# Kernel tuning notes

Measured on AMD Instinct MI355X. Metric: run time of the kernel, lower is better.

## Reference

```python
import jax, jax.numpy as jnp
import numpy as np

N_NODES = 100000


def sage_conv(x, src, dst, W_l, W_r, b):
    """PyG SAGEConv with mean aggregation: lin_l(mean_{j in N(i)} x_j) + lin_r(x_i) + b."""
    n = x.shape[0]
    msg = jax.ops.segment_sum(x[src], dst, num_segments=n)          # [N, C] sum of neighbor feats
    deg = jax.ops.segment_sum(jnp.ones_like(src, dtype=x.dtype), dst, num_segments=n)  # [N]
    agg = msg / jnp.maximum(deg, 1.0)[:, None]                      # mean aggregate
    return agg @ W_l + x @ W_r + b


def setup_inputs() -> dict:
    key = jax.random.key(0)
    ks = jax.random.split(key, 10)
    in_ch, hid, out_ch = 128, 128, 1
    E = 640000
    scale_in = 1.0 / np.sqrt(in_ch)
    scale_h = 1.0 / np.sqrt(hid)
    return {
        "x": jax.random.normal(ks[0], (N_NODES, in_ch), dtype=jnp.float32),
        "edge_index": jax.random.randint(ks[1], (2, E), 0, N_NODES, dtype=jnp.int64),
        "W1l": jax.random.normal(ks[2], (in_ch, hid), dtype=jnp.float32) * scale_in,
        "W1r": jax.random.normal(ks[3], (in_ch, hid), dtype=jnp.float32) * scale_in,
        "b1": jnp.zeros((hid,), dtype=jnp.float32),
        "W2l": jax.random.normal(ks[4], (hid, hid), dtype=jnp.float32) * scale_h,
        "W2r": jax.random.normal(ks[5], (hid, hid), dtype=jnp.float32) * scale_h,
        "b2": jnp.zeros((hid,), dtype=jnp.float32),
        "Wfc": jax.random.normal(ks[6], (hid, out_ch), dtype=jnp.float32) * scale_h,
        "bfc": jnp.zeros((out_ch,), dtype=jnp.float32),
    }


def reference(x, edge_index, W1l, W1r, b1, W2l, W2r, b2, Wfc, bfc):
    src, dst = edge_index[0], edge_index[1]
    h = sage_conv(x, src, dst, W1l, W1r, b1)
    h = jax.nn.relu(h)
    # dropout p=0.2 is identity in eval mode (training=False)
    h = sage_conv(h, src, dst, W2l, W2r, b2)
    h = jax.nn.relu(h)
    return jax.nn.sigmoid(h @ Wfc + bfc)
```

## Files before the change

### kernel.cpp

```cpp
#include <hip/hip_runtime.h>
#include <cstdint>

#define NN 100000
#define CH 128
#define NT_BLK 32
#define SCAN_B 256

typedef __bf16 bf16x8 __attribute__((ext_vector_type(8)));
typedef __bf16 bf16x4 __attribute__((ext_vector_type(4)));
typedef float  f32x4  __attribute__((ext_vector_type(4)));

__device__ __forceinline__ float b2f(unsigned short u) {
    union { unsigned int i; float f; } v; v.i = ((unsigned int)u) << 16; return v.f;
}


__global__ void k_count(const int* __restrict__ dst, int* __restrict__ cnt, int E) {
    int e = blockIdx.x * blockDim.x + threadIdx.x;
    if (e < E) atomicAdd(&cnt[dst[e]], 1);
}

__global__ void k_scan_block(const int* __restrict__ cnt, int* __restrict__ rowptr,
                             int* __restrict__ bsum, int n) {
    __shared__ int tmp[SCAN_B];
    int i = blockIdx.x * SCAN_B + threadIdx.x;
    int v = (i < n) ? cnt[i] : 0;
    tmp[threadIdx.x] = v;
    __syncthreads();
    for (int off = 1; off < SCAN_B; off <<= 1) {
        int t = (threadIdx.x >= off) ? tmp[threadIdx.x - off] : 0;
        __syncthreads();
        tmp[threadIdx.x] += t;
        __syncthreads();
    }
    if (i < n) rowptr[i] = tmp[threadIdx.x] - v;
    if (threadIdx.x == SCAN_B - 1) bsum[blockIdx.x] = tmp[SCAN_B - 1];
}

__global__ void k_scan_add(int* __restrict__ rowptr, const int* __restrict__ bsum,
                           int* __restrict__ cursor, int n, int E) {
    __shared__ int sd[SCAN_B];
    const int t = threadIdx.x;
    int s = 0;
    for (int j = t; j < (int)blockIdx.x; j += SCAN_B) s += bsum[j];
    sd[t] = s;
    __syncthreads();
    for (int off = SCAN_B / 2; off > 0; off >>= 1) {
        if (t < off) sd[t] += sd[t + off];
        __syncthreads();
    }
    const int base = sd[0];
    int i = blockIdx.x * SCAN_B + t;
    if (i < n) {
        int v = rowptr[i] + base;
        rowptr[i] = v;
        cursor[i] = v;
    }
    if (i == 0) rowptr[n] = E;
}

__global__ void k_fill(const int* __restrict__ src, const int* __restrict__ dst,
                       int* __restrict__ cursor, int* __restrict__ csr, int E) {
    int e = blockIdx.x * blockDim.x + threadIdx.x;
    if (e >= E) return;
    int slot = atomicAdd(&cursor[dst[e]], 1);
    csr[slot] = src[e];
}

__global__ void k_wconv(const float* __restrict__ W1l, const float* __restrict__ W1r,
                        const float* __restrict__ W2l, const float* __restrict__ W2r,
                        __bf16* __restrict__ wB) {
    int tid = blockIdx.x * blockDim.x + threadIdx.x;
    int l    = tid >> 12;
    int rem  = tid & 4095;
    int kt   = rem >> 9;
    int nt   = (rem >> 6) & 7;
    int lane = rem & 63;
    const float* Wl = l ? W2l : W1l;
    const float* Wr = l ? W2r : W1r;
    int n  = nt * 16 + (lane & 15);
    int k0 = kt * 32 + (lane >> 4) * 8;
    bf16x8 v;
#pragma unroll
    for (int i = 0; i < 8; ++i) {
        int k = k0 + i;
        float f = (k < CH) ? Wl[k * CH + n] : Wr[(k - CH) * CH + n];
        v[i] = (__bf16)f;
    }
    *reinterpret_cast<bf16x8*>(wB + (size_t)tid * 8) = v;
}

template<bool FC, typename FT>
__global__ __launch_bounds__(256) void k_layer(
    const FT* __restrict__ feat,
    const int* __restrict__ rowptr, const int* __restrict__ csr,
    const bf16x8* __restrict__ wfrag,
    const float* __restrict__ bias,
    const float* __restrict__ Wfc, const float* __restrict__ bfc,
    void* __restrict__ outv)
{
    __shared__ unsigned short a_lds[NT_BLK * 256];
    __shared__ float red[4][16];
    char* lb = (char*)a_lds;
    const int tid = threadIdx.x;
    const int node0 = blockIdx.x * NT_BLK;

    const int g = tid >> 5;
    const int q = tid & 31;

    auto loadrow = [&](int idx) -> float4 {
        if constexpr (sizeof(FT) == 2) {
            const ushort4 u = *reinterpret_cast<const ushort4*>(
                (const unsigned short*)feat + (size_t)idx * CH + q * 4);
            return make_float4(b2f(u.x), b2f(u.y), b2f(u.z), b2f(u.w));
        } else {
            return *reinterpret_cast<const float4*>((const float*)feat + (size_t)idx * CH + q * 4);
        }
    };

#pragma unroll
    for (int it = 0; it < NT_BLK / 8; ++it) {
        const int r = it * 8 + g;
        const int node = node0 + r;
        const int swz = (r & 7) << 4;
        float4 s = make_float4(0.f, 0.f, 0.f, 0.f);
        bf16x4 k2 = {(__bf16)0.f, (__bf16)0.f, (__bf16)0.f, (__bf16)0.f};
        if (node < NN) {
            const int r0 = rowptr[node], r1 = rowptr[node + 1];
            int rr = r0;
            for (; rr + 4 <= r1; rr += 4) {
                const int i0 = csr[rr], i1 = csr[rr + 1], i2 = csr[rr + 2], i3 = csr[rr + 3];
                const float4 v0 = loadrow(i0), v1 = loadrow(i1), v2 = loadrow(i2), v3 = loadrow(i3);
                s.x += (v0.x + v1.x) + (v2.x + v3.x);
                s.y += (v0.y + v1.y) + (v2.y + v3.y);
                s.z += (v0.z + v1.z) + (v2.z + v3.z);
                s.w += (v0.w + v1.w) + (v2.w + v3.w);
            }
            for (; rr < r1; ++rr) {
                const float4 v = loadrow(csr[rr]);
                s.x += v.x; s.y += v.y; s.z += v.z; s.w += v.w;
            }
            const float invd = 1.0f / fmaxf((float)(r1 - r0), 1.0f);
            s.x *= invd; s.y *= invd; s.z *= invd; s.w *= invd;
            if constexpr (sizeof(FT) == 2) {
                const ushort4 u = *reinterpret_cast<const ushort4*>(
                    (const unsigned short*)feat + (size_t)node * CH + q * 4);
                k2 = *reinterpret_cast<const bf16x4*>(&u);
            } else {
                const float4 sv = *reinterpret_cast<const float4*>((const float*)feat + (size_t)node * CH + q * 4);
                k2[0] = (__bf16)sv.x; k2[1] = (__bf16)sv.y; k2[2] = (__bf16)sv.z; k2[3] = (__bf16)sv.w;
            }
        }
        bf16x4 a;
        a[0] = (__bf16)s.x; a[1] = (__bf16)s.y; a[2] = (__bf16)s.z; a[3] = (__bf16)s.w;
        *reinterpret_cast<bf16x4*>(lb + r * 512 + ((q * 8) ^ swz)) = a;
        *reinterpret_cast<bf16x4*>(lb + r * 512 + ((256 + q * 8) ^ swz)) = k2;
    }
    __syncthreads();

    const int lane = tid & 63;
    const int w = tid >> 6;
    const int rows16 = (w >> 1) * 16;
    const int ntbase = (w & 1) * 4;
    const int row = rows16 + (lane & 15);
    const int rswz = (row & 7) << 4;
    const int abase = row * 512;
    const int asub = (lane >> 4) * 16;

    f32x4 acc[4];
#pragma unroll
    for (int nt = 0; nt < 4; ++nt) { acc[nt][0] = 0.f; acc[nt][1] = 0.f; acc[nt][2] = 0.f; acc[nt][3] = 0.f; }

#pragma unroll
    for (int kt = 0; kt < 8; ++kt) {
        const bf16x8 a = *reinterpret_cast<const bf16x8*>(lb + abase + ((kt * 64 + asub) ^ rswz));
        const bf16x8* bp = wfrag + kt * 512 + ntbase * 64 + lane;
#pragma unroll
        for (int nt = 0; nt < 4; ++nt) {
            const bf16x8 b = bp[nt * 64];
            acc[nt] = __builtin_amdgcn_mfma_f32_16x16x32_bf16(a, b, acc[nt], 0, 0, 0);
        }
    }

    const int nbase = lane & 15;
    if (!FC) {
        __bf16* out = (__bf16*)outv;
#pragma unroll
        for (int nt = 0; nt < 4; ++nt) {
            const int ch = (ntbase + nt) * 16 + nbase;
            const float bv = bias[ch];
#pragma unroll
            for (int rr = 0; rr < 4; ++rr) {
                const int node = node0 + rows16 + (lane >> 4) * 4 + rr;
                if (node < NN)
                    out[(size_t)node * CH + ch] = (__bf16)fmaxf(acc[nt][rr] + bv, 0.0f);
            }
        }
    } else {
        float* out = (float*)outv;
        float p[4] = {0.f, 0.f, 0.f, 0.f};
#pragma unroll
        for (int nt = 0; nt < 4; ++nt) {
            const int ch = (ntbase + nt) * 16 + nbase;
            const float bv = bias[ch];
            const float wf = Wfc[ch];
#pragma unroll
            for (int rr = 0; rr < 4; ++rr)
                p[rr] += fmaxf(acc[nt][rr] + bv, 0.0f) * wf;
        }
#pragma unroll
        for (int m = 1; m < 16; m <<= 1) {
#pragma unroll
            for (int rr = 0; rr < 4; ++rr) p[rr] += __shfl_xor(p[rr], m);
        }
        if (nbase == 0) {
#pragma unroll
            for (int rr = 0; rr < 4; ++rr)
                red[w][(lane >> 4) * 4 + rr] = p[rr];
        }
        __syncthreads();
        if (tid < NT_BLK) {
            const int rloc = tid;
            const float z = (rloc < 16 ? red[0][rloc] + red[1][rloc]
                                       : red[2][rloc - 16] + red[3][rloc - 16]) + bfc[0];
            const int node = node0 + rloc;
            if (node < NN) out[node] = 1.0f / (1.0f + expf(-z));
        }
    }
}


extern "C" void kernel_launch(void* const* d_in, const int* in_sizes, int n_in,
                              void* d_out, int out_size, void* d_ws, size_t ws_size,
                              hipStream_t stream) {
    const float* x   = (const float*)d_in[0];
    const int*   ei  = (const int*)d_in[1];
    const float* W1l = (const float*)d_in[2];
    const float* W1r = (const float*)d_in[3];
    const float* b1  = (const float*)d_in[4];
    const float* W2l = (const float*)d_in[5];
    const float* W2r = (const float*)d_in[6];
    const float* b2  = (const float*)d_in[7];
    const float* Wfc = (const float*)d_in[8];
    const float* bfc = (const float*)d_in[9];

    const int E = in_sizes[1] / 2;
    const int* src = ei;
    const int* dst = ei + E;

    unsigned short* h1 = (unsigned short*)d_ws;
    __bf16* wB     = (__bf16*)(h1 + (size_t)NN * CH);
    int*    cnt    = (int*)(wB + 65536);
    int*    rowptr = cnt + NN;
    int*    bsum   = rowptr + NN + 1;
    int*    csr    = bsum + 512;

    const int nb = (NN + SCAN_B - 1) / SCAN_B;

    hipMemsetAsync(cnt, 0, (size_t)NN * sizeof(int), stream);
    k_count<<<(E + 255) / 256, 256, 0, stream>>>(dst, cnt, E);
    k_scan_block<<<nb, SCAN_B, 0, stream>>>(cnt, rowptr, bsum, NN);
    k_scan_add<<<nb, SCAN_B, 0, stream>>>(rowptr, bsum, cnt, NN, E);
    k_fill<<<(E + 255) / 256, 256, 0, stream>>>(src, dst, cnt, csr, E);

    k_wconv<<<32, 256, 0, stream>>>(W1l, W1r, W2l, W2r, wB);

    const int blocks = (NN + NT_BLK - 1) / NT_BLK;
    k_layer<false, float><<<blocks, 256, 0, stream>>>(
        x, rowptr, csr, (const bf16x8*)wB, b1, Wfc, bfc, h1);
    k_layer<true, unsigned short><<<blocks, 256, 0, stream>>>(
        h1, rowptr, csr, (const bf16x8*)(wB + 32768), b2, Wfc, bfc, d_out);
}
```

Baseline: 294.5 us.

## Fuse scan passes and weight conversion into one launch; mask gather tail

Merges the two-pass block scan and the weight bf16 conversion into a single kernel. Each scan block now computes its own base by summing every preceding count directly, which removes two launches and the bsum buffer. The cost is redundant work: later blocks re-read up to the whole count array, quadratic in total but small at 100k nodes. The gather loop also drops its scalar remainder loop and processes neighbours four at a time, clamping indices and zeroing extra loads with masks, which avoids the divergent tail but issues wasted loads for partial groups.

```diff
diff --git a/kernel.cpp b/kernel.cpp
--- a/kernel.cpp
+++ b/kernel.cpp
@@ -20,29 +20,37 @@
     if (e < E) atomicAdd(&cnt[dst[e]], 1);
 }
 
-__global__ void k_scan_block(const int* __restrict__ cnt, int* __restrict__ rowptr,
-                             int* __restrict__ bsum, int n) {
-    __shared__ int tmp[SCAN_B];
-    int i = blockIdx.x * SCAN_B + threadIdx.x;
-    int v = (i < n) ? cnt[i] : 0;
-    tmp[threadIdx.x] = v;
-    __syncthreads();
-    for (int off = 1; off < SCAN_B; off <<= 1) {
-        int t = (threadIdx.x >= off) ? tmp[threadIdx.x - off] : 0;
-        __syncthreads();
-        tmp[threadIdx.x] += t;
-        __syncthreads();
-    }
-    if (i < n) rowptr[i] = tmp[threadIdx.x] - v;
-    if (threadIdx.x == SCAN_B - 1) bsum[blockIdx.x] = tmp[SCAN_B - 1];
-}
-
-__global__ void k_scan_add(int* __restrict__ rowptr, const int* __restrict__ bsum,
-                           int* __restrict__ cursor, int n, int E) {
+__global__ void k_scan_wconv(const int* __restrict__ cnt, int* __restrict__ rowptr,
+                             int* __restrict__ cursor, int n, int E, int nb,
+                             const float* __restrict__ W1l, const float* __restrict__ W1r,
+                             const float* __restrict__ W2l, const float* __restrict__ W2r,
+                             __bf16* __restrict__ wB) {
+    const int t = threadIdx.x;
+    if ((int)blockIdx.x >= nb) {
+        int tid = ((int)blockIdx.x - nb) * SCAN_B + t;
+        int l    = tid >> 12;
+        int rem  = tid & 4095;
+        int kt   = rem >> 9;
+        int nt   = (rem >> 6) & 7;
+        int lane = rem & 63;
+        const float* Wl = l ? W2l : W1l;
+        const float* Wr = l ? W2r : W1r;
+        int nn = nt * 16 + (lane & 15);
+        int k0 = kt * 32 + (lane >> 4) * 8;
+        bf16x8 v;
+#pragma unroll
+        for (int i = 0; i < 8; ++i) {
+            int k = k0 + i;
+            float f = (k < CH) ? Wl[k * CH + nn] : Wr[(k - CH) * CH + nn];
+            v[i] = (__bf16)f;
+        }
+        *reinterpret_cast<bf16x8*>(wB + (size_t)tid * 8) = v;
+        return;
+    }
     __shared__ int sd[SCAN_B];
-    const int t = threadIdx.x;
+    const int lim = (int)blockIdx.x * SCAN_B;
     int s = 0;
-    for (int j = t; j < (int)blockIdx.x; j += SCAN_B) s += bsum[j];
+    for (int j = t; j < lim; j += SCAN_B) s += cnt[j];
     sd[t] = s;
     __syncthreads();
     for (int off = SCAN_B / 2; off > 0; off >>= 1) {
@@ -50,11 +58,21 @@
         __syncthreads();
     }
     const int base = sd[0];
-    int i = blockIdx.x * SCAN_B + t;
+    __syncthreads();
+    const int i = lim + t;
+    const int v = (i < n) ? cnt[i] : 0;
+    sd[t] = v;
+    __syncthreads();
+    for (int off = 1; off < SCAN_B; off <<= 1) {
+        int tv = (t >= off) ? sd[t - off] : 0;
+        __syncthreads();
+        sd[t] += tv;
+        __syncthreads();
+    }
     if (i < n) {
-        int v = rowptr[i] + base;
-        rowptr[i] = v;
-        cursor[i] = v;
+        const int excl = sd[t] - v + base;
+        rowptr[i] = excl;
+        cursor[i] = excl;
     }
     if (i == 0) rowptr[n] = E;
 }
@@ -65,29 +83,6 @@
     if (e >= E) return;
     int slot = atomicAdd(&cursor[dst[e]], 1);
     csr[slot] = src[e];
-}
-
-__global__ void k_wconv(const float* __restrict__ W1l, const float* __restrict__ W1r,
-                        const float* __restrict__ W2l, const float* __restrict__ W2r,
-                        __bf16* __restrict__ wB) {
-    int tid = blockIdx.x * blockDim.x + threadIdx.x;
-    int l    = tid >> 12;
-    int rem  = tid & 4095;
-    int kt   = rem >> 9;
-    int nt   = (rem >> 6) & 7;
-    int lane = rem & 63;
-    const float* Wl = l ? W2l : W1l;
-    const float* Wr = l ? W2r : W1r;
-    int n  = nt * 16 + (lane & 15);
-    int k0 = kt * 32 + (lane >> 4) * 8;
-    bf16x8 v;
-#pragma unroll
-    for (int i = 0; i < 8; ++i) {
-        int k = k0 + i;
-        float f = (k < CH) ? Wl[k * CH + n] : Wr[(k - CH) * CH + n];
-        v[i] = (__bf16)f;
-    }
-    *reinterpret_cast<bf16x8*>(wB + (size_t)tid * 8) = v;
 }
 
 template<bool FC, typename FT>
@@ -127,18 +122,20 @@
         bf16x4 k2 = {(__bf16)0.f, (__bf16)0.f, (__bf16)0.f, (__bf16)0.f};
         if (node < NN) {
             const int r0 = rowptr[node], r1 = rowptr[node + 1];
-            int rr = r0;
-            for (; rr + 4 <= r1; rr += 4) {
-                const int i0 = csr[rr], i1 = csr[rr + 1], i2 = csr[rr + 2], i3 = csr[rr + 3];
+            const int last = r1 - 1;
+            for (int rr = r0; rr < r1; rr += 4) {
+                const int i0 = csr[rr];
+                const int i1 = csr[min(rr + 1, last)];
+                const int i2 = csr[min(rr + 2, last)];
+                const int i3 = csr[min(rr + 3, last)];
+                const float m1 = (rr + 1 < r1) ? 1.f : 0.f;
+                const float m2 = (rr + 2 < r1) ? 1.f : 0.f;
+                const float m3 = (rr + 3 < r1) ? 1.f : 0.f;
                 const float4 v0 = loadrow(i0), v1 = loadrow(i1), v2 = loadrow(i2), v3 = loadrow(i3);
-                s.x += (v0.x + v1.x) + (v2.x + v3.x);
-                s.y += (v0.y + v1.y) + (v2.y + v3.y);
-                s.z += (v0.z + v1.z) + (v2.z + v3.z);
-                s.w += (v0.w + v1.w) + (v2.w + v3.w);
-            }
-            for (; rr < r1; ++rr) {
-                const float4 v = loadrow(csr[rr]);
-                s.x += v.x; s.y += v.y; s.z += v.z; s.w += v.w;
+                s.x += v0.x + m1 * v1.x + m2 * v2.x + m3 * v3.x;
+                s.y += v0.y + m1 * v1.y + m2 * v2.y + m3 * v3.y;
+                s.z += v0.z + m1 * v1.z + m2 * v2.z + m3 * v3.z;
+                s.w += v0.w + m1 * v1.w + m2 * v2.w + m3 * v3.w;
             }
             const float invd = 1.0f / fmaxf((float)(r1 - r0), 1.0f);
             s.x *= invd; s.y *= invd; s.z *= invd; s.w *= invd;
@@ -251,19 +248,17 @@
     unsigned short* h1 = (unsigned short*)d_ws;
     __bf16* wB     = (__bf16*)(h1 + (size_t)NN * CH);
     int*    cnt    = (int*)(wB + 65536);
-    int*    rowptr = cnt + NN;
-    int*    bsum   = rowptr + NN + 1;
-    int*    csr    = bsum + 512;
+    int*    cur    = cnt + NN;
+    int*    rowptr = cur + NN;
+    int*    csr    = rowptr + NN + 1;
 
     const int nb = (NN + SCAN_B - 1) / SCAN_B;
 
     hipMemsetAsync(cnt, 0, (size_t)NN * sizeof(int), stream);
     k_count<<<(E + 255) / 256, 256, 0, stream>>>(dst, cnt, E);
-    k_scan_block<<<nb, SCAN_B, 0, stream>>>(cnt, rowptr, bsum, NN);
-    k_scan_add<<<nb, SCAN_B, 0, stream>>>(rowptr, bsum, cnt, NN, E);
-    k_fill<<<(E + 255) / 256, 256, 0, stream>>>(src, dst, cnt, csr, E);
-
-    k_wconv<<<32, 256, 0, stream>>>(W1l, W1r, W2l, W2r, wB);
+    k_scan_wconv<<<nb + 32, SCAN_B, 0, stream>>>(cnt, rowptr, cur, NN, E, nb,
+                                                 W1l, W1r, W2l, W2r, wB);
+    k_fill<<<(E + 255) / 256, 256, 0, stream>>>(src, dst, cur, csr, E);
 
     const int blocks = (NN + NT_BLK - 1) / NT_BLK;
     k_layer<false, float><<<blocks, 256, 0, stream>>>(
```

New measurement: 330.1 us. 1.12x slower.

## Pre-convert x to bf16, fuse setup kernels, batch gather loads by eight

Applied to the files above, without the earlier changes.

Converts x to bf16 up front inside the edge-count kernel so layer 1 gathers half as many bytes per neighbor. The weight conversion is merged into the scan kernel to cut a launch. The neighbor loop now issues eight masked gathers per iteration, clamping indices to the last edge, so more loads are in flight. The cost is an extra full pass over x plus more workspace, and low-degree nodes now do redundant masked loads.

```diff
diff --git a/kernel.cpp b/kernel.cpp
--- a/kernel.cpp
+++ b/kernel.cpp
@@ -14,27 +14,66 @@
     union { unsigned int i; float f; } v; v.i = ((unsigned int)u) << 16; return v.f;
 }
 
-
-__global__ void k_count(const int* __restrict__ dst, int* __restrict__ cnt, int E) {
-    int e = blockIdx.x * blockDim.x + threadIdx.x;
-    if (e < E) atomicAdd(&cnt[dst[e]], 1);
-}
-
-__global__ void k_scan_block(const int* __restrict__ cnt, int* __restrict__ rowptr,
-                             int* __restrict__ bsum, int n) {
+__global__ void k_count_xconv(const int* __restrict__ dst, int* __restrict__ cnt, int E,
+                              const float* __restrict__ x, unsigned short* __restrict__ xb,
+                              int cb) {
+    const int b = blockIdx.x;
+    if (b < cb) {
+        int e = b * 256 + threadIdx.x;
+        if (e < E) atomicAdd(&cnt[dst[e]], 1);
+        return;
+    }
+    const size_t base = ((size_t)(b - cb) * 256 + threadIdx.x) * 8;
+    if (base < (size_t)NN * CH) {
+        const float4 a = *reinterpret_cast<const float4*>(x + base);
+        const float4 c = *reinterpret_cast<const float4*>(x + base + 4);
+        bf16x8 o;
+        o[0] = (__bf16)a.x; o[1] = (__bf16)a.y; o[2] = (__bf16)a.z; o[3] = (__bf16)a.w;
+        o[4] = (__bf16)c.x; o[5] = (__bf16)c.y; o[6] = (__bf16)c.z; o[7] = (__bf16)c.w;
+        *reinterpret_cast<bf16x8*>(xb + base) = o;
+    }
+}
+
+__global__ void k_scan_wb(const int* __restrict__ cnt, int* __restrict__ rowptr,
+                          int* __restrict__ bsum, int n, int nb,
+                          const float* __restrict__ W1l, const float* __restrict__ W1r,
+                          const float* __restrict__ W2l, const float* __restrict__ W2r,
+                          __bf16* __restrict__ wB) {
+    const int t = threadIdx.x;
+    if ((int)blockIdx.x >= nb) {
+        int tid = ((int)blockIdx.x - nb) * SCAN_B + t;
+        int l    = tid >> 12;
+        int rem  = tid & 4095;
+        int kt   = rem >> 9;
+        int nt   = (rem >> 6) & 7;
+        int lane = rem & 63;
+        const float* Wl = l ? W2l : W1l;
+        const float* Wr = l ? W2r : W1r;
+        int nn = nt * 16 + (lane & 15);
+        int k0 = kt * 32 + (lane >> 4) * 8;
+        bf16x8 v;
+#pragma unroll
+        for (int i = 0; i < 8; ++i) {
+            int k = k0 + i;
+            float f = (k < CH) ? Wl[k * CH + nn] : Wr[(k - CH) * CH + nn];
+            v[i] = (__bf16)f;
+        }
+        *reinterpret_cast<bf16x8*>(wB + (size_t)tid * 8) = v;
+        return;
+    }
     __shared__ int tmp[SCAN_B];
-    int i = blockIdx.x * SCAN_B + threadIdx.x;
+    int i = blockIdx.x * SCAN_B + t;
     int v = (i < n) ? cnt[i] : 0;
-    tmp[threadIdx.x] = v;
+    tmp[t] = v;
     __syncthreads();
     for (int off = 1; off < SCAN_B; off <<= 1) {
-        int t = (threadIdx.x >= off) ? tmp[threadIdx.x - off] : 0;
-        __syncthreads();
-        tmp[threadIdx.x] += t;
-        __syncthreads();
-    }
-    if (i < n) rowptr[i] = tmp[threadIdx.x] - v;
-    if (threadIdx.x == SCAN_B - 1) bsum[blockIdx.x] = tmp[SCAN_B - 1];
+        int tv = (t >= off) ? tmp[t - off] : 0;
+        __syncthreads();
+        tmp[t] += tv;
+        __syncthreads();
+    }
+    if (i < n) rowptr[i] = tmp[t] - v;
+    if (t == SCAN_B - 1) bsum[blockIdx.x] = tmp[SCAN_B - 1];
 }
 
 __global__ void k_scan_add(int* __restrict__ rowptr, const int* __restrict__ bsum,
@@ -67,32 +106,9 @@
     csr[slot] = src[e];
 }
 
-__global__ void k_wconv(const float* __restrict__ W1l, const float* __restrict__ W1r,
-                        const float* __restrict__ W2l, const float* __restrict__ W2r,
-                        __bf16* __restrict__ wB) {
-    int tid = blockIdx.x * blockDim.x + threadIdx.x;
-    int l    = tid >> 12;
-    int rem  = tid & 4095;
-    int kt   = rem >> 9;
-    int nt   = (rem >> 6) & 7;
-    int lane = rem & 63;
-    const float* Wl = l ? W2l : W1l;
-    const float* Wr = l ? W2r : W1r;
-    int n  = nt * 16 + (lane & 15);
-    int k0 = kt * 32 + (lane >> 4) * 8;
-    bf16x8 v;
-#pragma unroll
-    for (int i = 0; i < 8; ++i) {
-        int k = k0 + i;
-        float f = (k < CH) ? Wl[k * CH + n] : Wr[(k - CH) * CH + n];
-        v[i] = (__bf16)f;
-    }
-    *reinterpret_cast<bf16x8*>(wB + (size_t)tid * 8) = v;
-}
-
-template<bool FC, typename FT>
+template<bool FC>
 __global__ __launch_bounds__(256) void k_layer(
-    const FT* __restrict__ feat,
+    const unsigned short* __restrict__ feat,
     const int* __restrict__ rowptr, const int* __restrict__ csr,
     const bf16x8* __restrict__ wfrag,
     const float* __restrict__ bias,
@@ -108,16 +124,6 @@
     const int g = tid >> 5;
     const int q = tid & 31;
 
-    auto loadrow = [&](int idx) -> float4 {
-        if constexpr (sizeof(FT) == 2) {
-            const ushort4 u = *reinterpret_cast<const ushort4*>(
-                (const unsigned short*)feat + (size_t)idx * CH + q * 4);
-            return make_float4(b2f(u.x), b2f(u.y), b2f(u.z), b2f(u.w));
-        } else {
-            return *reinterpret_cast<const float4*>((const float*)feat + (size_t)idx * CH + q * 4);
-        }
-    };
-
 #pragma unroll
     for (int it = 0; it < NT_BLK / 8; ++it) {
         const int r = it * 8 + g;
@@ -127,29 +133,29 @@
         bf16x4 k2 = {(__bf16)0.f, (__bf16)0.f, (__bf16)0.f, (__bf16)0.f};
         if (node < NN) {
             const int r0 = rowptr[node], r1 = rowptr[node + 1];
-            int rr = r0;
-            for (; rr + 4 <= r1; rr += 4) {
-                const int i0 = csr[rr], i1 = csr[rr + 1], i2 = csr[rr + 2], i3 = csr[rr + 3];
-                const float4 v0 = loadrow(i0), v1 = loadrow(i1), v2 = loadrow(i2), v3 = loadrow(i3);
-                s.x += (v0.x + v1.x) + (v2.x + v3.x);
-                s.y += (v0.y + v1.y) + (v2.y + v3.y);
-                s.z += (v0.z + v1.z) + (v2.z + v3.z);
-                s.w += (v0.w + v1.w) + (v2.w + v3.w);
-            }
-            for (; rr < r1; ++rr) {
-                const float4 v = loadrow(csr[rr]);
-                s.x += v.x; s.y += v.y; s.z += v.z; s.w += v.w;
+            const int last = r1 - 1;
+            for (int rr = r0; rr < r1; rr += 8) {
+                ushort4 uv[8];
+                float mk[8];
+#pragma unroll
+                for (int u = 0; u < 8; ++u) {
+                    const int p = rr + u;
+                    const int idx = csr[p <= last ? p : last];
+                    uv[u] = *reinterpret_cast<const ushort4*>(feat + (size_t)idx * CH + q * 4);
+                    mk[u] = (p < r1) ? 1.f : 0.f;
+                }
+#pragma unroll
+                for (int u = 0; u < 8; ++u) {
+                    s.x += mk[u] * b2f(uv[u].x);
+                    s.y += mk[u] * b2f(uv[u].y);
+                    s.z += mk[u] * b2f(uv[u].z);
+                    s.w += mk[u] * b2f(uv[u].w);
+                }
             }
             const float invd = 1.0f / fmaxf((float)(r1 - r0), 1.0f);
             s.x *= invd; s.y *= invd; s.z *= invd; s.w *= invd;
-            if constexpr (sizeof(FT) == 2) {
-                const ushort4 u = *reinterpret_cast<const ushort4*>(
-                    (const unsigned short*)feat + (size_t)node * CH + q * 4);
-                k2 = *reinterpret_cast<const bf16x4*>(&u);
-            } else {
-                const float4 sv = *reinterpret_cast<const float4*>((const float*)feat + (size_t)node * CH + q * 4);
-                k2[0] = (__bf16)sv.x; k2[1] = (__bf16)sv.y; k2[2] = (__bf16)sv.z; k2[3] = (__bf16)sv.w;
-            }
+            const ushort4 u = *reinterpret_cast<const ushort4*>(feat + (size_t)node * CH + q * 4);
+            k2 = *reinterpret_cast<const bf16x4*>(&u);
         }
         bf16x4 a;
         a[0] = (__bf16)s.x; a[1] = (__bf16)s.y; a[2] = (__bf16)s.z; a[3] = (__bf16)s.w;
@@ -249,25 +255,28 @@
     const int* dst = ei + E;
 
     unsigned short* h1 = (unsigned short*)d_ws;
-    __bf16* wB     = (__bf16*)(h1 + (size_t)NN * CH);
+    unsigned short* xb = h1 + (size_t)NN * CH;
+    __bf16* wB     = (__bf16*)(xb + (size_t)NN * CH);
     int*    cnt    = (int*)(wB + 65536);
-    int*    rowptr = cnt + NN;
+    int*    cur    = cnt + NN;
+    int*    rowptr = cur + NN;
     int*    bsum   = rowptr + NN + 1;
     int*    csr    = bsum + 512;
 
     const int nb = (NN + SCAN_B - 1) / SCAN_B;
+    const int cb = (E + 255) / 256;
+    const int xcb = (NN * CH) / 2048;
 
     hipMemsetAsync(cnt, 0, (size_t)NN * sizeof(int), stream);
-    k_count<<<(E + 255) / 256, 256, 0, stream>>>(dst, cnt, E);
-    k_scan_block<<<nb, SCAN_B, 0, stream>>>(cnt, rowptr, bsum, NN);
-    k_scan_add<<<nb, SCAN_B, 0, stream>>>(rowptr, bsum, cnt, NN, E);
-    k_fill<<<(E + 255) / 256, 256, 0, stream>>>(src, dst, cnt, csr, E);
-
-    k_wconv<<<32, 256, 0, stream>>>(W1l, W1r, W2l, W2r, wB);
+    k_count_xconv<<<cb + xcb, 256, 0, stream>>>(dst, cnt, E, x, xb, cb);
+    k_scan_wb<<<nb + 32, SCAN_B, 0, stream>>>(cnt, rowptr, bsum, NN, nb,
+                                              W1l, W1r, W2l, W2r, wB);
+    k_scan_add<<<nb, SCAN_B, 0, stream>>>(rowptr, bsum, cur, NN, E);
+    k_fill<<<cb, 256, 0, stream>>>(src, dst, cur, csr, E);
 
     const int blocks = (NN + NT_BLK - 1) / NT_BLK;
-    k_layer<false, float><<<blocks, 256, 0, stream>>>(
-        x, rowptr, csr, (const bf16x8*)wB, b1, Wfc, bfc, h1);
-    k_layer<true, unsigned short><<<blocks, 256, 0, stream>>>(
+    k_layer<false><<<blocks, 256, 0, stream>>>(
+        xb, rowptr, csr, (const bf16x8*)wB, b1, Wfc, bfc, h1);
+    k_layer<true><<<blocks, 256, 0, stream>>>(
         h1, rowptr, csr, (const bf16x8*)(wB + 32768), b2, Wfc, bfc, d_out);
 }
```

After: 263.7 us. -10.5%, faster.
